# Kernel tuning notes

Measured on AMD Instinct MI355X. Metric: run time of the kernel, lower is better.

Reference implementation:

```python
import jax, jax.numpy as jnp
import numpy as np

EMBED_DIM = 256
NUM_HEADS = 8
NUM_LEVELS = 4
NUM_POINTS = 4
HEAD_DIM = EMBED_DIM // NUM_HEADS


def _bilinear_sample(img, x, y):
    """img: [N,C,H,W]; x,y: [N,P] absolute pixel coords (align_corners=False mapping
    already applied by caller). Zero padding outside, matching F.grid_sample."""
    N, C, H, W = img.shape
    x0 = jnp.floor(x)
    y0 = jnp.floor(y)
    wx1 = x - x0
    wy1 = y - y0
    img_flat = img.reshape(N, C, H * W)

    def gather(ix, iy):
        valid = ((ix >= 0) & (ix <= W - 1) & (iy >= 0) & (iy <= H - 1)).astype(img.dtype)
        idx = (jnp.clip(iy, 0, H - 1) * W + jnp.clip(ix, 0, W - 1)).astype(jnp.int32)
        v = jnp.take_along_axis(img_flat, idx[:, None, :], axis=2)  # [N,C,P]
        return v * valid[:, None, :]

    return (gather(x0, y0) * ((1.0 - wx1) * (1.0 - wy1))[:, None, :]
            + gather(x0 + 1.0, y0) * (wx1 * (1.0 - wy1))[:, None, :]
            + gather(x0, y0 + 1.0) * ((1.0 - wx1) * wy1)[:, None, :]
            + gather(x0 + 1.0, y0 + 1.0) * (wx1 * wy1)[:, None, :])


def _reference_points(H, W):
    yy, xx = jnp.meshgrid(jnp.arange(H, dtype=jnp.float32), jnp.arange(W, dtype=jnp.float32), indexing='ij')
    # stack order is (x, y), matching grid_sample's (x=width, y=height) convention
    return jnp.stack([(xx + 0.5) / W, (yy + 0.5) / H], axis=-1).reshape(H * W, 2)


def _frame_attention(q_feat, values, level_shapes, Wq, bq, Woff, boff, Wattn, battn, Wout, bout):
    Bt, C, H, W = q_feat.shape
    N = H * W
    q = q_feat.reshape(Bt, C, N).transpose(0, 2, 1) @ Wq + bq  # [Bt,N,C]
    off = (q @ Woff + boff).reshape(Bt, N, NUM_HEADS, NUM_LEVELS, NUM_POINTS, 2)
    aw = jax.nn.softmax((q @ Wattn + battn).reshape(Bt, N, NUM_HEADS, NUM_LEVELS * NUM_POINTS), axis=-1)
    aw = aw.reshape(Bt, N, NUM_HEADS, NUM_LEVELS, NUM_POINTS)
    ref = _reference_points(H, W)  # [N,2]
    sampled = []
    for l, (val, (Hl, Wl)) in enumerate(zip(values, level_shapes)):
        loc = ref[None, :, None, None, :] + off[:, :, :, l] / jnp.array([Wl, Hl], dtype=q.dtype)
        grid = jnp.clip(loc, 0.0, 1.0) * 2.0 - 1.0  # [Bt,N,M,K,2]
        grid = grid.transpose(0, 2, 1, 3, 4).reshape(Bt * NUM_HEADS, N * NUM_POINTS, 2)
        # align_corners=False: pixel = ((g+1)*size - 1)/2
        x = ((grid[..., 0] + 1.0) * Wl - 1.0) * 0.5
        y = ((grid[..., 1] + 1.0) * Hl - 1.0) * 0.5
        s = _bilinear_sample(val, x, y)  # [Bt*M, hd, N*K]
        s = s.reshape(Bt, NUM_HEADS, HEAD_DIM, N, NUM_POINTS).transpose(0, 3, 1, 4, 2)  # [Bt,N,M,K,hd]
        sampled.append(s)
    samp = jnp.stack(sampled, axis=3)  # [Bt,N,M,L,K,hd]
    out = (samp * aw[..., None]).sum(axis=(3, 4)).reshape(Bt, N, C)
    out = out @ Wout + bout
    return out.transpose(0, 2, 1).reshape(Bt, C, H, W)


def _forward(feats, Wq, bq, Wv, bv, Woff, boff, Wattn, battn, Wout, bout):
    B, C, H0, W0, T = feats[0].shape
    # original loops over frames t; frames are independent, so fold T into batch
    feats_bt = [jnp.moveaxis(f, -1, 1).reshape(f.shape[0] * T, C, f.shape[2], f.shape[3]) for f in feats]
    level_shapes = [(f.shape[2], f.shape[3]) for f in feats_bt]
    Bt = B * T
    # value projection per level (identical across query scales; compute once)
    values = []
    for f, (Hl, Wl) in zip(feats_bt, level_shapes):
        v = f.reshape(Bt, C, Hl * Wl).transpose(0, 2, 1) @ Wv + bv  # [Bt,HW,C]
        v = v.reshape(Bt, Hl * Wl, NUM_HEADS, HEAD_DIM).transpose(0, 2, 3, 1).reshape(Bt * NUM_HEADS, HEAD_DIM, Hl, Wl)
        values.append(v)
    outs = []
    for f, (Hl, Wl) in zip(feats_bt, level_shapes):
        o = _frame_attention(f, values, level_shapes, Wq, bq, Woff, boff, Wattn, battn, Wout, bout)
        outs.append(o.reshape(B, T, C, Hl, Wl).transpose(0, 2, 3, 4, 1))  # back to [B,C,H,W,T]
    return tuple(outs)


def setup_inputs() -> dict:
    key = jax.random.key(0)
    ks = jax.random.split(key, 10)
    B, T, C = 2, 2, EMBED_DIM
    shapes = [(64, 64), (32, 32), (16, 16), (8, 8)]
    inp = {}
    for i, (H, W) in enumerate(shapes):
        inp[f"feats{i}"] = jax.random.normal(ks[i], (B, C, H, W, T), dtype=jnp.float32)
    s = float(1.0 / np.sqrt(C))
    noff = NUM_HEADS * NUM_LEVELS * NUM_POINTS
    inp["Wq"] = jax.random.normal(ks[4], (C, C), jnp.float32) * s
    inp["bq"] = jnp.zeros((C,), jnp.float32)
    inp["Wv"] = jax.random.normal(ks[5], (C, C), jnp.float32) * s
    inp["bv"] = jnp.zeros((C,), jnp.float32)
    inp["Woff"] = jax.random.normal(ks[6], (C, noff * 2), jnp.float32) * 0.01
    inp["boff"] = jax.random.normal(ks[7], (noff * 2,), jnp.float32) * 2.0
    inp["Wattn"] = jax.random.normal(ks[8], (C, noff), jnp.float32) * 0.01
    inp["battn"] = jnp.zeros((noff,), jnp.float32)
    inp["Wout"] = jax.random.normal(ks[9], (C, C), jnp.float32) * s
    inp["bout"] = jnp.zeros((C,), jnp.float32)
    return inp


def reference(feats0, feats1, feats2, feats3, Wq, bq, Wv, bv, Woff, boff, Wattn, battn, Wout, bout):
    return _forward([feats0, feats1, feats2, feats3], Wq, bq, Wv, bv, Woff, boff, Wattn, battn, Wout, bout)
```

## Files before the change

### kernel.cpp

```cpp
#include <hip/hip_runtime.h>
#include <hip/hip_bf16.h>

#define NR 21760

typedef short short8 __attribute__((ext_vector_type(8)));
typedef float f32x4 __attribute__((ext_vector_type(4)));

__device__ __forceinline__ int level_of_row(int R) {
    if (R < 16384) return 0;
    if (R < 20480) return 1;
    if (R < 21504) return 2;
    return 3;
}

__device__ __forceinline__ unsigned pk2(float a, float b) {
    __hip_bfloat16 x = __float2bfloat16(a), y = __float2bfloat16(b);
    return (unsigned)*(unsigned short*)&x | ((unsigned)*(unsigned short*)&y << 16);
}

__global__ __launch_bounds__(256) void pack_all_kernel(const float* __restrict__ f0,
                                                       const float* __restrict__ f1,
                                                       const float* __restrict__ f2,
                                                       const float* __restrict__ f3,
                                                       __hip_bfloat16* __restrict__ XP) {
    int bx = blockIdx.x;
    const float* f; int nj, Wl, rowbase, rel;
    if (bx < 1024)      { f = f0; nj = 128; Wl = 64; rowbase = 0;     rel = bx; }
    else if (bx < 1280) { f = f1; nj = 32;  Wl = 32; rowbase = 16384; rel = bx - 1024; }
    else if (bx < 1344) { f = f2; nj = 8;   Wl = 16; rowbase = 20480; rel = bx - 1280; }
    else                { f = f3; nj = 2;   Wl = 8;  rowbase = 21504; rel = bx - 1344; }
    const int HW = Wl * Wl;
    const int HWT = HW * 2;
    const int j0 = (rel % nj) * 64;
    const int c0 = ((rel / nj) & 3) * 64;
    const int b  = rel / (nj * 4);
    const int tid = threadIdx.x;
    __shared__ float tile[64][65];
    {
        const int cl = tid >> 2, q = tid & 3;
        const float* fb = f + (size_t)(b * 256 + c0 + cl) * HWT + j0 + q * 16;
#pragma unroll
        for (int k = 0; k < 4; ++k) {
            float4 v = *(const float4*)(fb + k * 4);
            *(float4*)(&tile[cl][q * 16 + k * 4]) = v;
        }
    }
    __syncthreads();
    {
        const int jl = tid >> 4, cq = tid & 15;
#pragma unroll
        for (int pass = 0; pass < 4; ++pass) {
            int jloc = pass * 16 + jl;
            int j = j0 + jloc;
            int p = j >> 1, t = j & 1;
            int row = rowbase + (b * 2 + t) * HW + p;
            float v0 = tile[cq * 4 + 0][jloc];
            float v1 = tile[cq * 4 + 1][jloc];
            float v2 = tile[cq * 4 + 2][jloc];
            float v3 = tile[cq * 4 + 3][jloc];
            uint2 o;
            o.x = pk2(v0, v1); o.y = pk2(v2, v3);
            *(uint2*)(&XP[(size_t)row * 256 + c0 + cq * 4]) = o;
        }
    }
}

__global__ __launch_bounds__(256) void wtrans_all_kernel(const float* __restrict__ Wq,
                                                         const float* __restrict__ Wv,
                                                         const float* __restrict__ Woff,
                                                         const float* __restrict__ Wattn,
                                                         const float* __restrict__ Wout,
                                                         const float* __restrict__ bq,
                                                         const float* __restrict__ boff,
                                                         const float* __restrict__ battn,
                                                         __hip_bfloat16* __restrict__ WTvo,
                                                         __hip_bfloat16* __restrict__ WToa,
                                                         __hip_bfloat16* __restrict__ Wqb,
                                                         __hip_bfloat16* __restrict__ WTout,
                                                         float* __restrict__ bias_oa) {
    const int bx = blockIdx.x;
    const int tid = threadIdx.x;
    if (bx == 256) {
        {
            int n = tid;
            float s = 0.f;
            for (int j = 0; j < 256; ++j) s += bq[j] * Woff[(size_t)j * 256 + n];
            bias_oa[n] = s + boff[n];
        }
        if (tid < 128) {
            int n = tid;
            float s = 0.f;
            for (int j = 0; j < 256; ++j) s += bq[j] * Wattn[(size_t)j * 128 + n];
            bias_oa[256 + n] = s + battn[n];
        }
        return;
    }
    if (bx >= 160 && bx < 192) {
        int e0 = (bx - 160) * 2048 + tid * 8;
        float4 a = *(const float4*)(Wq + e0);
        float4 b = *(const float4*)(Wq + e0 + 4);
        uint4 o;
        o.x = pk2(a.x, a.y); o.y = pk2(a.z, a.w);
        o.z = pk2(b.x, b.y); o.w = pk2(b.z, b.w);
        *(uint4*)(&Wqb[e0]) = o;
        return;
    }
    __shared__ float t[32][33];
    const float* W; __hip_bfloat16* WT; int N; int rel;
    if (bx < 64)       { W = Wv;    WT = WTvo;             N = 256; rel = bx; }
    else if (bx < 128) { W = Woff;  WT = WToa;             N = 256; rel = bx - 64; }
    else if (bx < 160) { W = Wattn; WT = WToa + 256 * 256; N = 128; rel = bx - 128; }
    else               { W = Wout;  WT = WTout;            N = 256; rel = bx - 192; }
    const int K = 256;
    const int ntiles = N >> 5;
    const int n0 = (rel % ntiles) * 32, k0 = (rel / ntiles) * 32;
    const int c = tid & 31, r = tid >> 5;
#pragma unroll
    for (int i = 0; i < 4; ++i)
        t[r + 8 * i][c] = W[(size_t)(k0 + r + 8 * i) * N + n0 + c];
    __syncthreads();
#pragma unroll
    for (int i = 0; i < 4; ++i)
        WT[(size_t)(n0 + r + 8 * i) * K + k0 + c] = __float2bfloat16(t[c][r + 8 * i]);
}

template <int OUTMODE>
__global__ __launch_bounds__(256) void gemm_mfma(const __hip_bfloat16* __restrict__ A,
                                                 const __hip_bfloat16* __restrict__ BT,
                                                 const float* __restrict__ bias,
                                                 const float* __restrict__ bias2,
                                                 void* __restrict__ Cout,
                                                 void* __restrict__ Cout2,
                                                 int M, int N, int K) {
    __shared__ __align__(16) __hip_bfloat16 As[64][72];
    __shared__ __align__(16) __hip_bfloat16 Bs[64][72];
    const int m0 = blockIdx.x * 64;
    const int n0 = blockIdx.y * 64;
    const int w = threadIdx.x >> 6;
    const int lane = threadIdx.x & 63;
    const int wm = (w >> 1) * 32;
    const int wn = (w & 1) * 32;
    const int fr = lane & 15;
    const int fq = lane >> 4;
    const int srow = threadIdx.x >> 3;
    const int schunk = threadIdx.x & 7;
    f32x4 acc[2][2] = {};

    for (int kt = 0; kt < K; kt += 64) {
        __syncthreads();
#pragma unroll
        for (int i = 0; i < 2; ++i) {
            int r = srow + 32 * i;
            float4 va = *(const float4*)(&A[(size_t)(m0 + r) * K + kt + schunk * 8]);
            *(float4*)(&As[r][schunk * 8]) = va;
            float4 vb = *(const float4*)(&BT[(size_t)(n0 + r) * K + kt + schunk * 8]);
            *(float4*)(&Bs[r][schunk * 8]) = vb;
        }
        __syncthreads();
#pragma unroll
        for (int ks = 0; ks < 2; ++ks) {
            short8 a[2], b[2];
#pragma unroll
            for (int fi = 0; fi < 2; ++fi)
                a[fi] = *(const short8*)(&As[wm + fi * 16 + fr][ks * 32 + fq * 8]);
#pragma unroll
            for (int fj = 0; fj < 2; ++fj)
                b[fj] = *(const short8*)(&Bs[wn + fj * 16 + fr][ks * 32 + fq * 8]);
#pragma unroll
            for (int fi = 0; fi < 2; ++fi)
#pragma unroll
                for (int fj = 0; fj < 2; ++fj)
                    acc[fi][fj] = __builtin_amdgcn_mfma_f32_16x16x32_bf16(
                        a[fi], b[fj], acc[fi][fj], 0, 0, 0);
        }
    }

    if (OUTMODE == 4) {
        if (n0 < 256) {
            __hip_bfloat16* dst = (__hip_bfloat16*)Cout;
#pragma unroll
            for (int fi = 0; fi < 2; ++fi)
#pragma unroll
                for (int fj = 0; fj < 2; ++fj) {
                    int col = n0 + wn + fj * 16 + fr;
                    float bb = bias[col];
#pragma unroll
                    for (int r = 0; r < 4; ++r) {
                        int row = m0 + wm + fi * 16 + fq * 4 + r;
                        dst[(size_t)row * 256 + col] = __float2bfloat16(acc[fi][fj][r] + bb);
                    }
                }
        } else {
            float* dst = (float*)Cout2;
#pragma unroll
            for (int fi = 0; fi < 2; ++fi)
#pragma unroll
                for (int fj = 0; fj < 2; ++fj) {
                    int col = n0 - 256 + wn + fj * 16 + fr;
                    float bb = bias2[col];
#pragma unroll
                    for (int r = 0; r < 4; ++r) {
                        int row = m0 + wm + fi * 16 + fq * 4 + r;
                        dst[(size_t)row * 384 + col] = acc[fi][fj][r] + bb;
                    }
                }
        }
    } else {
#pragma unroll
        for (int fi = 0; fi < 2; ++fi)
#pragma unroll
            for (int fj = 0; fj < 2; ++fj) {
                int col = n0 + wn + fj * 16 + fr;
                float bb = bias ? bias[col] : 0.f;
#pragma unroll
                for (int r = 0; r < 4; ++r) {
                    int row = m0 + wm + fi * 16 + fq * 4 + r;
                    ((__hip_bfloat16*)Cout)[(size_t)row * N + col] =
                        __float2bfloat16(acc[fi][fj][r] + bb);
                }
            }
    }
}

__global__ __launch_bounds__(256) void gemm_scatter_kernel(const __hip_bfloat16* __restrict__ A,
                                                           const __hip_bfloat16* __restrict__ BT,
                                                           const float* __restrict__ bias,
                                                           float* __restrict__ out) {
    const int bx = blockIdx.x;
    int l, b, p0;
    if (bx < 256)      { l = 0; b = bx >> 7;          p0 = (bx & 127) * 32; }
    else if (bx < 320) { l = 1; b = (bx - 256) >> 5;  p0 = ((bx - 256) & 31) * 32; }
    else if (bx < 336) { l = 2; b = (bx - 320) >> 3;  p0 = ((bx - 320) & 7) * 32; }
    else               { l = 3; b = (bx - 336) >> 1;  p0 = ((bx - 336) & 1) * 32; }
    const int qbase[4]    = {0, 16384, 20480, 21504};
    const int hwtab[4]    = {4096, 1024, 256, 64};
    const size_t obase[4] = {0, 4194304, 5242880, 5505024};
    const int HW = hwtab[l];
    const int qb = qbase[l];

    __shared__ __align__(16) __hip_bfloat16 As[64][72];
    __shared__ __align__(16) __hip_bfloat16 Bs[64][72];
    const int n0 = blockIdx.y * 64;
    const int w = threadIdx.x >> 6;
    const int lane = threadIdx.x & 63;
    const int wm = (w >> 1) * 32;
    const int wn = (w & 1) * 32;
    const int fr = lane & 15;
    const int fq = lane >> 4;
    const int srow = threadIdx.x >> 3;
    const int schunk = threadIdx.x & 7;
    f32x4 acc[2][2] = {};

    for (int kt = 0; kt < 256; kt += 64) {
        __syncthreads();
#pragma unroll
        for (int i = 0; i < 2; ++i) {
            int m = srow + 32 * i;
            int t = (m >> 4) & 1;
            int pl = (m & 15) | ((m & 32) >> 1);
            int R = qb + (2 * b + t) * HW + p0 + pl;
            float4 va = *(const float4*)(&A[(size_t)R * 256 + kt + schunk * 8]);
            *(float4*)(&As[m][schunk * 8]) = va;
            float4 vb = *(const float4*)(&BT[(size_t)(n0 + m) * 256 + kt + schunk * 8]);
            *(float4*)(&Bs[m][schunk * 8]) = vb;
        }
        __syncthreads();
#pragma unroll
        for (int ks = 0; ks < 2; ++ks) {
            short8 a[2], bfr[2];
#pragma unroll
            for (int fi = 0; fi < 2; ++fi)
                a[fi] = *(const short8*)(&As[wm + fi * 16 + fr][ks * 32 + fq * 8]);
#pragma unroll
            for (int fj = 0; fj < 2; ++fj)
                bfr[fj] = *(const short8*)(&Bs[wn + fj * 16 + fr][ks * 32 + fq * 8]);
#pragma unroll
            for (int fi = 0; fi < 2; ++fi)
#pragma unroll
                for (int fj = 0; fj < 2; ++fj)
                    acc[fi][fj] = __builtin_amdgcn_mfma_f32_16x16x32_bf16(
                        a[fi], bfr[fj], acc[fi][fj], 0, 0, 0);
        }
    }
    const int plbase = fq * 4 + ((wm & 32) >> 1);
#pragma unroll
    for (int fj = 0; fj < 2; ++fj) {
        int col = n0 + wn + fj * 16 + fr;
        float bb = bias[col];
#pragma unroll
        for (int r = 0; r < 4; ++r) {
            int p = p0 + plbase + r;
            size_t addr = obase[l] + (((size_t)b * 256 + col) * HW + p) * 2;
            float2 v;
            v.x = acc[0][fj][r] + bb;
            v.y = acc[1][fj][r] + bb;
            *(float2*)(out + addr) = v;
        }
    }
}

__device__ __forceinline__ void acc8(f32x4& a, f32x4& b, uint4 v, float w) {
    a[0] = fmaf(w, __uint_as_float(v.x << 16),          a[0]);
    a[1] = fmaf(w, __uint_as_float(v.x & 0xffff0000u),  a[1]);
    a[2] = fmaf(w, __uint_as_float(v.y << 16),          a[2]);
    a[3] = fmaf(w, __uint_as_float(v.y & 0xffff0000u),  a[3]);
    b[0] = fmaf(w, __uint_as_float(v.z << 16),          b[0]);
    b[1] = fmaf(w, __uint_as_float(v.z & 0xffff0000u),  b[1]);
    b[2] = fmaf(w, __uint_as_float(v.w << 16),          b[2]);
    b[3] = fmaf(w, __uint_as_float(v.w & 0xffff0000u),  b[3]);
}

#define QB 4
__global__ __launch_bounds__(256, 2) void sample_kernel(const __hip_bfloat16* __restrict__ VAL,
                                                        const float* __restrict__ OA,
                                                        __hip_bfloat16* __restrict__ SAMP) {
    __shared__ __align__(16) int2 tapd[QB * 512];
    const int blk = blockIdx.x;
    const int work = (blk & 7) * 680 + (blk >> 3);
    const int R0 = work * QB;
    const int tid = threadIdx.x;
    const int qbase[4] = {0, 16384, 20480, 21504};
    const int wsh[4]   = {6, 5, 4, 3};
    const int hwsh[4]  = {12, 10, 8, 6};
    const float invwf[4] = {1.f/64.f, 1.f/32.f, 1.f/16.f, 1.f/8.f};

    if (tid < QB * 32) {
        const int qh = tid >> 2, part = tid & 3;
        const int q = qh >> 3, h = qh & 7;
        const int R = R0 + q;
        const int lq = level_of_row(R);
        const int r2 = R - qbase[lq];
        const int bt = r2 >> hwsh[lq];
        const int p  = r2 & ((1 << hwsh[lq]) - 1);
        const int pxi = p & ((1 << wsh[lq]) - 1);
        const int pyi = p >> wsh[lq];
        const float refx = (pxi + 0.5f) * invwf[lq];
        const float refy = (pyi + 0.5f) * invwf[lq];
        const float* oarow = OA + (size_t)R * 384;
        float4 offA = *(const float4*)(oarow + h * 32 + part * 8);
        float4 offB = *(const float4*)(oarow + h * 32 + part * 8 + 4);
        float4 awv  = *(const float4*)(oarow + 256 + h * 16 + part * 4);
        float m = fmaxf(fmaxf(awv.x, awv.y), fmaxf(awv.z, awv.w));
        m = fmaxf(m, __shfl_xor(m, 1));
        m = fmaxf(m, __shfl_xor(m, 2));
        float e0 = __expf(awv.x - m), e1 = __expf(awv.y - m);
        float e2 = __expf(awv.z - m), e3 = __expf(awv.w - m);
        float s = e0 + e1 + e2 + e3;
        s += __shfl_xor(s, 1);
        s += __shfl_xor(s, 2);
        const float inv = 1.0f / s;
        const int l = part;
        const int Wl = 1 << wsh[l];
        const float invWf = invwf[l];
        const int base = (qbase[l] + (bt << hwsh[l])) << 8;
        float oxy[8] = {offA.x, offA.y, offA.z, offA.w, offB.x, offB.y, offB.z, offB.w};
        float ee[4] = {e0, e1, e2, e3};
#pragma unroll
        for (int i = 0; i < 4; ++i) {
            float ox = oxy[2 * i], oy = oxy[2 * i + 1];
            float aw = ee[i] * inv;
            float lx = fminf(fmaxf(refx + ox * invWf, 0.f), 1.f);
            float ly = fminf(fmaxf(refy + oy * invWf, 0.f), 1.f);
            float px = lx * Wl - 0.5f;
            float py = ly * Wl - 0.5f;
            float x0f = floorf(px), y0f = floorf(py);
            int x0 = (int)x0f, y0 = (int)y0f;
            float wx = px - x0f, wy = py - y0f;
            float vx0 = (x0 >= 0) ? 1.f : 0.f;
            float vx1 = (x0 + 1 <= Wl - 1) ? 1.f : 0.f;
            float vy0 = (y0 >= 0) ? 1.f : 0.f;
            float vy1 = (y0 + 1 <= Wl - 1) ? 1.f : 0.f;
            int x0c = max(x0, 0), x1c = min(x0 + 1, Wl - 1);
            int y0c = max(y0, 0), y1c = min(y0 + 1, Wl - 1);
            int o00 = base + (((y0c << wsh[l]) + x0c) << 8);
            int o10 = base + (((y0c << wsh[l]) + x1c) << 8);
            int o01 = base + (((y1c << wsh[l]) + x0c) << 8);
            int o11 = base + (((y1c << wsh[l]) + x1c) << 8);
            float w00 = aw * (1.f - wx) * (1.f - wy) * vx0 * vy0;
            float w10 = aw * wx * (1.f - wy) * vx1 * vy0;
            float w01 = aw * (1.f - wx) * wy * vx0 * vy1;
            float w11 = aw * wx * wy * vx1 * vy1;
            int idx = ((q * 16 + part * 4 + i) * 8 + h) * 4;
            *(int4*)(&tapd[idx])     = make_int4(o00, __float_as_int(w00), o10, __float_as_int(w10));
            *(int4*)(&tapd[idx + 2]) = make_int4(o01, __float_as_int(w01), o11, __float_as_int(w11));
        }
    }
    __syncthreads();

    const int wq = tid >> 6, lane = tid & 63;
    const int u = lane >> 2, sub = lane & 3;
    const int c = u & 3, h4 = u >> 2;
    const int R = R0 + wq;
    const __hip_bfloat16* v0base = VAL + h4 * 32 + sub * 8;
    const __hip_bfloat16* v1base = VAL + (h4 + 4) * 32 + sub * 8;
    const int2* tp = &tapd[wq * 512];
    f32x4 aA0 = {0,0,0,0}, aA1 = {0,0,0,0};
    f32x4 aB0 = {0,0,0,0}, aB1 = {0,0,0,0};
#pragma unroll 2
    for (int t = 0; t < 16; ++t) {
        int2 d0 = tp[(t * 8 + h4) * 4 + c];
        int2 d1 = tp[(t * 8 + h4 + 4) * 4 + c];
        uint4 x0 = *(const uint4*)(v0base + d0.x);
        uint4 x1 = *(const uint4*)(v1base + d1.x);
        acc8(aA0, aA1, x0, __int_as_float(d0.y));
        acc8(aB0, aB1, x1, __int_as_float(d1.y));
    }
#pragma unroll
    for (int i = 0; i < 4; ++i) {
        aA0[i] += __shfl_xor(aA0[i], 4); aA0[i] += __shfl_xor(aA0[i], 8);
        aA1[i] += __shfl_xor(aA1[i], 4); aA1[i] += __shfl_xor(aA1[i], 8);
        aB0[i] += __shfl_xor(aB0[i], 4); aB0[i] += __shfl_xor(aB0[i], 8);
        aB1[i] += __shfl_xor(aB1[i], 4); aB1[i] += __shfl_xor(aB1[i], 8);
    }
    if (c == 0) {
        uint4 o0, o1;
        o0.x = pk2(aA0[0], aA0[1]); o0.y = pk2(aA0[2], aA0[3]);
        o0.z = pk2(aA1[0], aA1[1]); o0.w = pk2(aA1[2], aA1[3]);
        o1.x = pk2(aB0[0], aB0[1]); o1.y = pk2(aB0[2], aB0[3]);
        o1.z = pk2(aB1[0], aB1[1]); o1.w = pk2(aB1[2], aB1[3]);
        *(uint4*)(&SAMP[(size_t)R * 256 + h4 * 32 + sub * 8]) = o0;
        *(uint4*)(&SAMP[(size_t)R * 256 + (h4 + 4) * 32 + sub * 8]) = o1;
    }
}

extern "C" void kernel_launch(void* const* d_in, const int* in_sizes, int n_in,
                              void* d_out, int out_size, void* d_ws, size_t ws_size,
                              hipStream_t stream) {
    (void)in_sizes; (void)n_in; (void)out_size; (void)ws_size;
    const float* f0 = (const float*)d_in[0];
    const float* f1 = (const float*)d_in[1];
    const float* f2 = (const float*)d_in[2];
    const float* f3 = (const float*)d_in[3];
    const float* Wq    = (const float*)d_in[4];
    const float* bq    = (const float*)d_in[5];
    const float* Wv    = (const float*)d_in[6];
    const float* bv    = (const float*)d_in[7];
    const float* Woff  = (const float*)d_in[8];
    const float* boff  = (const float*)d_in[9];
    const float* Wattn = (const float*)d_in[10];
    const float* battn = (const float*)d_in[11];
    const float* Wout  = (const float*)d_in[12];
    const float* bout  = (const float*)d_in[13];
    float* out = (float*)d_out;

    char* w = (char*)d_ws;
    __hip_bfloat16* XPb   = (__hip_bfloat16*)w;   w += (size_t)NR * 256 * 2;
    __hip_bfloat16* SAMPb = (__hip_bfloat16*)w;   w += (size_t)NR * 256 * 2;
    __hip_bfloat16* VAL   = (__hip_bfloat16*)w;   w += (size_t)NR * 256 * 2;
    float* OA   = (float*)w;                      w += (size_t)NR * 384 * 4;
    __hip_bfloat16* WTvo  = (__hip_bfloat16*)w;   w += 640 * 256 * 2;
    __hip_bfloat16* WToa  = (__hip_bfloat16*)w;   w += 384 * 256 * 2;
    __hip_bfloat16* Wqb   = (__hip_bfloat16*)w;   w += 256 * 256 * 2;
    __hip_bfloat16* WTout = (__hip_bfloat16*)w;   w += 256 * 256 * 2;
    float* bias_oa = (float*)w;                   w += 384 * 4;

    hipLaunchKernelGGL(pack_all_kernel, dim3(1360), dim3(256), 0, stream, f0, f1, f2, f3, XPb);

    hipLaunchKernelGGL(wtrans_all_kernel, dim3(257), dim3(256), 0, stream,
                       Wq, Wv, Woff, Wattn, Wout, bq, boff, battn,
                       WTvo, WToa, Wqb, WTout, bias_oa);

    hipLaunchKernelGGL((gemm_mfma<3>), dim3(6, 4), dim3(256), 0, stream,
                       WToa, Wqb, nullptr, nullptr, (void*)(WTvo + 256 * 256), nullptr,
                       384, 256, 256);

    hipLaunchKernelGGL((gemm_mfma<4>), dim3(NR / 64, 10), dim3(256), 0, stream,
                       XPb, WTvo, bv, bias_oa, (void*)VAL, (void*)OA, NR, 640, 256);

    hipLaunchKernelGGL(sample_kernel, dim3(NR / QB), dim3(256), 0, stream, VAL, OA, SAMPb);

    hipLaunchKernelGGL(gemm_scatter_kernel, dim3(340, 4), dim3(256), 0, stream,
                       SAMPb, WTout, bout, out);
}
```

Measured before the change: 105.3 us.

## Fold Wq product into weight prep and use 128x128 tiles for dual GEMM

The small weight-product GEMM (Wq times Woff/Wattn) is now computed with scalar fp32 FMAs inside the weight-transpose kernel, which removes one kernel launch and the intermediate bf16 buffers. The main value/offset projection GEMM moves from 64x64 to 128x128 block tiles with 4x4 MFMA fragments per wave, raising data reuse per load at the cost of more registers and fewer blocks (170x5). The sample kernel also drops its interleaved block-to-work mapping in favour of a linear one, which may change cache locality.

```diff
diff --git a/kernel.cpp b/kernel.cpp
--- a/kernel.cpp
+++ b/kernel.cpp
@@ -74,13 +74,11 @@
                                                          const float* __restrict__ boff,
                                                          const float* __restrict__ battn,
                                                          __hip_bfloat16* __restrict__ WTvo,
-                                                         __hip_bfloat16* __restrict__ WToa,
-                                                         __hip_bfloat16* __restrict__ Wqb,
                                                          __hip_bfloat16* __restrict__ WTout,
                                                          float* __restrict__ bias_oa) {
     const int bx = blockIdx.x;
     const int tid = threadIdx.x;
-    if (bx == 256) {
+    if (bx == 224) {
         {
             int n = tid;
             float s = 0.f;
@@ -95,130 +93,111 @@
         }
         return;
     }
-    if (bx >= 160 && bx < 192) {
-        int e0 = (bx - 160) * 2048 + tid * 8;
-        float4 a = *(const float4*)(Wq + e0);
-        float4 b = *(const float4*)(Wq + e0 + 4);
-        uint4 o;
-        o.x = pk2(a.x, a.y); o.y = pk2(a.z, a.w);
-        o.z = pk2(b.x, b.y); o.w = pk2(b.z, b.w);
-        *(uint4*)(&Wqb[e0]) = o;
+    if (bx >= 128) {
+        const int rel = bx - 128;
+        const int n0 = (rel % 12) * 32, k0 = (rel / 12) * 32;
+        const int n = tid & 31, kt = tid >> 5;
+        const int nn = n0 + n;
+        float acc[4] = {0.f, 0.f, 0.f, 0.f};
+        for (int j = 0; j < 256; ++j) {
+            float wo = (nn < 256) ? Woff[(size_t)j * 256 + nn]
+                                  : Wattn[(size_t)j * 128 + nn - 256];
+#pragma unroll
+            for (int i = 0; i < 4; ++i)
+                acc[i] += wo * Wq[(size_t)(k0 + kt * 4 + i) * 256 + j];
+        }
+#pragma unroll
+        for (int i = 0; i < 4; ++i)
+            WTvo[(size_t)(256 + nn) * 256 + k0 + kt * 4 + i] = __float2bfloat16(acc[i]);
         return;
     }
     __shared__ float t[32][33];
-    const float* W; __hip_bfloat16* WT; int N; int rel;
-    if (bx < 64)       { W = Wv;    WT = WTvo;             N = 256; rel = bx; }
-    else if (bx < 128) { W = Woff;  WT = WToa;             N = 256; rel = bx - 64; }
-    else if (bx < 160) { W = Wattn; WT = WToa + 256 * 256; N = 128; rel = bx - 128; }
-    else               { W = Wout;  WT = WTout;            N = 256; rel = bx - 192; }
-    const int K = 256;
-    const int ntiles = N >> 5;
-    const int n0 = (rel % ntiles) * 32, k0 = (rel / ntiles) * 32;
+    const float* W = (bx < 64) ? Wv : Wout;
+    __hip_bfloat16* WT = (bx < 64) ? WTvo : WTout;
+    const int rel = bx & 63;
+    const int n0 = (rel % 8) * 32, k0 = (rel / 8) * 32;
     const int c = tid & 31, r = tid >> 5;
 #pragma unroll
     for (int i = 0; i < 4; ++i)
-        t[r + 8 * i][c] = W[(size_t)(k0 + r + 8 * i) * N + n0 + c];
+        t[r + 8 * i][c] = W[(size_t)(k0 + r + 8 * i) * 256 + n0 + c];
     __syncthreads();
 #pragma unroll
     for (int i = 0; i < 4; ++i)
-        WT[(size_t)(n0 + r + 8 * i) * K + k0 + c] = __float2bfloat16(t[c][r + 8 * i]);
-}
-
-template <int OUTMODE>
-__global__ __launch_bounds__(256) void gemm_mfma(const __hip_bfloat16* __restrict__ A,
-                                                 const __hip_bfloat16* __restrict__ BT,
-                                                 const float* __restrict__ bias,
-                                                 const float* __restrict__ bias2,
-                                                 void* __restrict__ Cout,
-                                                 void* __restrict__ Cout2,
-                                                 int M, int N, int K) {
-    __shared__ __align__(16) __hip_bfloat16 As[64][72];
-    __shared__ __align__(16) __hip_bfloat16 Bs[64][72];
-    const int m0 = blockIdx.x * 64;
-    const int n0 = blockIdx.y * 64;
+        WT[(size_t)(n0 + r + 8 * i) * 256 + k0 + c] = __float2bfloat16(t[c][r + 8 * i]);
+}
+
+__global__ __launch_bounds__(256) void gemm128_dual(const __hip_bfloat16* __restrict__ A,
+                                                    const __hip_bfloat16* __restrict__ BT,
+                                                    const float* __restrict__ bias,
+                                                    const float* __restrict__ bias2,
+                                                    __hip_bfloat16* __restrict__ VAL,
+                                                    float* __restrict__ OA) {
+    __shared__ __align__(16) __hip_bfloat16 As[128][72];
+    __shared__ __align__(16) __hip_bfloat16 Bs[128][72];
+    const int m0 = blockIdx.x * 128;
+    const int n0 = blockIdx.y * 128;
     const int w = threadIdx.x >> 6;
     const int lane = threadIdx.x & 63;
-    const int wm = (w >> 1) * 32;
-    const int wn = (w & 1) * 32;
+    const int wm = (w >> 1) * 64;
+    const int wn = (w & 1) * 64;
     const int fr = lane & 15;
     const int fq = lane >> 4;
     const int srow = threadIdx.x >> 3;
     const int schunk = threadIdx.x & 7;
-    f32x4 acc[2][2] = {};
-
-    for (int kt = 0; kt < K; kt += 64) {
+    f32x4 acc[4][4] = {};
+
+    for (int kt = 0; kt < 256; kt += 64) {
         __syncthreads();
 #pragma unroll
-        for (int i = 0; i < 2; ++i) {
+        for (int i = 0; i < 4; ++i) {
             int r = srow + 32 * i;
-            float4 va = *(const float4*)(&A[(size_t)(m0 + r) * K + kt + schunk * 8]);
+            float4 va = *(const float4*)(&A[(size_t)(m0 + r) * 256 + kt + schunk * 8]);
             *(float4*)(&As[r][schunk * 8]) = va;
-            float4 vb = *(const float4*)(&BT[(size_t)(n0 + r) * K + kt + schunk * 8]);
+            float4 vb = *(const float4*)(&BT[(size_t)(n0 + r) * 256 + kt + schunk * 8]);
             *(float4*)(&Bs[r][schunk * 8]) = vb;
         }
         __syncthreads();
 #pragma unroll
         for (int ks = 0; ks < 2; ++ks) {
-            short8 a[2], b[2];
-#pragma unroll
-            for (int fi = 0; fi < 2; ++fi)
+            short8 a[4], b[4];
+#pragma unroll
+            for (int fi = 0; fi < 4; ++fi)
                 a[fi] = *(const short8*)(&As[wm + fi * 16 + fr][ks * 32 + fq * 8]);
 #pragma unroll
-            for (int fj = 0; fj < 2; ++fj)
+            for (int fj = 0; fj < 4; ++fj)
                 b[fj] = *(const short8*)(&Bs[wn + fj * 16 + fr][ks * 32 + fq * 8]);
 #pragma unroll
-            for (int fi = 0; fi < 2; ++fi)
-#pragma unroll
-                for (int fj = 0; fj < 2; ++fj)
+            for (int fi = 0; fi < 4; ++fi)
+#pragma unroll
+                for (int fj = 0; fj < 4; ++fj)
                     acc[fi][fj] = __builtin_amdgcn_mfma_f32_16x16x32_bf16(
                         a[fi], b[fj], acc[fi][fj], 0, 0, 0);
         }
     }
 
-    if (OUTMODE == 4) {
-        if (n0 < 256) {
-            __hip_bfloat16* dst = (__hip_bfloat16*)Cout;
-#pragma unroll
-            for (int fi = 0; fi < 2; ++fi)
-#pragma unroll
-                for (int fj = 0; fj < 2; ++fj) {
-                    int col = n0 + wn + fj * 16 + fr;
-                    float bb = bias[col];
-#pragma unroll
-                    for (int r = 0; r < 4; ++r) {
-                        int row = m0 + wm + fi * 16 + fq * 4 + r;
-                        dst[(size_t)row * 256 + col] = __float2bfloat16(acc[fi][fj][r] + bb);
-                    }
+#pragma unroll
+    for (int fj = 0; fj < 4; ++fj) {
+        int col = n0 + wn + fj * 16 + fr;
+        if (col < 256) {
+            float bb = bias[col];
+#pragma unroll
+            for (int fi = 0; fi < 4; ++fi)
+#pragma unroll
+                for (int r = 0; r < 4; ++r) {
+                    int row = m0 + wm + fi * 16 + fq * 4 + r;
+                    VAL[(size_t)row * 256 + col] = __float2bfloat16(acc[fi][fj][r] + bb);
                 }
         } else {
-            float* dst = (float*)Cout2;
-#pragma unroll
-            for (int fi = 0; fi < 2; ++fi)
-#pragma unroll
-                for (int fj = 0; fj < 2; ++fj) {
-                    int col = n0 - 256 + wn + fj * 16 + fr;
-                    float bb = bias2[col];
-#pragma unroll
-                    for (int r = 0; r < 4; ++r) {
-                        int row = m0 + wm + fi * 16 + fq * 4 + r;
-                        dst[(size_t)row * 384 + col] = acc[fi][fj][r] + bb;
-                    }
-                }
-        }
-    } else {
-#pragma unroll
-        for (int fi = 0; fi < 2; ++fi)
-#pragma unroll
-            for (int fj = 0; fj < 2; ++fj) {
-                int col = n0 + wn + fj * 16 + fr;
-                float bb = bias ? bias[col] : 0.f;
+            int c2 = col - 256;
+            float bb = bias2[c2];
+#pragma unroll
+            for (int fi = 0; fi < 4; ++fi)
 #pragma unroll
                 for (int r = 0; r < 4; ++r) {
                     int row = m0 + wm + fi * 16 + fq * 4 + r;
-                    ((__hip_bfloat16*)Cout)[(size_t)row * N + col] =
-                        __float2bfloat16(acc[fi][fj][r] + bb);
+                    OA[(size_t)row * 384 + c2] = acc[fi][fj][r] + bb;
                 }
-            }
+        }
     }
 }
 
@@ -315,9 +294,7 @@
                                                         const float* __restrict__ OA,
                                                         __hip_bfloat16* __restrict__ SAMP) {
     __shared__ __align__(16) int2 tapd[QB * 512];
-    const int blk = blockIdx.x;
-    const int work = (blk & 7) * 680 + (blk >> 3);
-    const int R0 = work * QB;
+    const int R0 = blockIdx.x * QB;
     const int tid = threadIdx.x;
     const int qbase[4] = {0, 16384, 20480, 21504};
     const int wsh[4]   = {6, 5, 4, 3};
@@ -449,23 +426,17 @@
     __hip_bfloat16* VAL   = (__hip_bfloat16*)w;   w += (size_t)NR * 256 * 2;
     float* OA   = (float*)w;                      w += (size_t)NR * 384 * 4;
     __hip_bfloat16* WTvo  = (__hip_bfloat16*)w;   w += 640 * 256 * 2;
-    __hip_bfloat16* WToa  = (__hip_bfloat16*)w;   w += 384 * 256 * 2;
-    __hip_bfloat16* Wqb   = (__hip_bfloat16*)w;   w += 256 * 256 * 2;
     __hip_bfloat16* WTout = (__hip_bfloat16*)w;   w += 256 * 256 * 2;
     float* bias_oa = (float*)w;                   w += 384 * 4;
 
     hipLaunchKernelGGL(pack_all_kernel, dim3(1360), dim3(256), 0, stream, f0, f1, f2, f3, XPb);
 
-    hipLaunchKernelGGL(wtrans_all_kernel, dim3(257), dim3(256), 0, stream,
+    hipLaunchKernelGGL(wtrans_all_kernel, dim3(225), dim3(256), 0, stream,
                        Wq, Wv, Woff, Wattn, Wout, bq, boff, battn,
-                       WTvo, WToa, Wqb, WTout, bias_oa);
-
-    hipLaunchKernelGGL((gemm_mfma<3>), dim3(6, 4), dim3(256), 0, stream,
-                       WToa, Wqb, nullptr, nullptr, (void*)(WTvo + 256 * 256), nullptr,
-                       384, 256, 256);
-
-    hipLaunchKernelGGL((gemm_mfma<4>), dim3(NR / 64, 10), dim3(256), 0, stream,
-                       XPb, WTvo, bv, bias_oa, (void*)VAL, (void*)OA, NR, 640, 256);
+                       WTvo, WTout, bias_oa);
+
+    hipLaunchKernelGGL(gemm128_dual, dim3(NR / 128, 5), dim3(256), 0, stream,
+                       XPb, WTvo, bv, bias_oa, VAL, OA);
 
     hipLaunchKernelGGL(sample_kernel, dim3(NR / QB), dim3(256), 0, stream, VAL, OA, SAMPb);
 
```

Result: slower. 117.3 us (+11.4%).
